# Kernel optimization log

Measured on AMD Instinct MI355X. Metric: run time of the kernel, lower is better.

Reference implementation:

```python
import jax, jax.numpy as jnp
import numpy as np

B, H, W = 8, 64, 64
DIM, NH, WS = 384, 6, 14
HD = DIM // NH
MLP = int(DIM * 4.0)
EPS = 1e-5
SCALE = HD ** -0.5


def setup_inputs() -> dict:
    key = jax.random.key(0)
    ks = jax.random.split(key, 8)
    init = lambda k, shape: (jax.random.normal(k, shape, dtype=jnp.float32) * 0.02)
    return {
        "x": jax.random.normal(ks[0], (B, H, W, DIM), dtype=jnp.float32),
        "ln1_w": jnp.ones((DIM,), jnp.float32),
        "ln1_b": jnp.zeros((DIM,), jnp.float32),
        "qkv_w": init(ks[1], (DIM, 3 * DIM)),
        "qkv_b": jnp.zeros((3 * DIM,), jnp.float32),
        "proj_w": init(ks[2], (DIM, DIM)),
        "proj_b": jnp.zeros((DIM,), jnp.float32),
        "rel_pos_h": init(ks[3], (2 * WS - 1, HD)),
        "rel_pos_w": init(ks[4], (2 * WS - 1, HD)),
        "ln2_w": jnp.ones((DIM,), jnp.float32),
        "ln2_b": jnp.zeros((DIM,), jnp.float32),
        "fc1_w": init(ks[5], (DIM, MLP)),
        "fc1_b": jnp.zeros((MLP,), jnp.float32),
        "fc2_w": init(ks[6], (MLP, DIM)),
        "fc2_b": jnp.zeros((DIM,), jnp.float32),
    }


def _layernorm(x, w, b):
    m = x.mean(-1, keepdims=True)
    v = ((x - m) ** 2).mean(-1, keepdims=True)
    return (x - m) * jax.lax.rsqrt(v + EPS) * w + b


def _get_rel_pos(rel_pos, ws):
    # q_size == k_size == ws and rel_pos has 2*ws-1 rows, so torch's
    # F.interpolate to max_rel_dist=2*ws-1 is an identity; direct indexing.
    coords = jnp.arange(ws)[:, None] - jnp.arange(ws)[None, :] + (ws - 1)
    return rel_pos[coords]  # (ws, ws, head_dim)


def _attention(xw, qkv_w, qkv_b, proj_w, proj_b, rel_pos_h, rel_pos_w):
    Bw = xw.shape[0]
    N = WS * WS
    qkv = xw.reshape(Bw, N, DIM) @ qkv_w + qkv_b  # (Bw, N, 3*DIM)
    qkv = qkv.reshape(Bw, N, 3, NH, HD).transpose(2, 0, 3, 1, 4).reshape(3, Bw * NH, N, HD)
    q, k, v = qkv[0], qkv[1], qkv[2]
    attn = jnp.einsum("bqd,bkd->bqk", q * SCALE, k)  # (Bw*NH, N, N)
    Rh = _get_rel_pos(rel_pos_h, WS)
    Rw = _get_rel_pos(rel_pos_w, WS)
    rq = q.reshape(Bw * NH, WS, WS, HD)
    rel_h = jnp.einsum("bhwc,hkc->bhwk", rq, Rh)
    rel_w = jnp.einsum("bhwc,wkc->bhwk", rq, Rw)
    attn = (attn.reshape(Bw * NH, WS, WS, WS, WS)
            + rel_h[:, :, :, :, None]
            + rel_w[:, :, :, None, :]).reshape(Bw * NH, N, N)
    attn = jax.nn.softmax(attn, axis=-1)
    out = jnp.einsum("bqk,bkd->bqd", attn, v)
    out = out.reshape(Bw, NH, WS, WS, HD).transpose(0, 2, 3, 1, 4).reshape(Bw, WS, WS, DIM)
    return out @ proj_w + proj_b


def reference(x, ln1_w, ln1_b, qkv_w, qkv_b, proj_w, proj_b, rel_pos_h, rel_pos_w,
              ln2_w, ln2_b, fc1_w, fc1_b, fc2_w, fc2_b):
    shortcut = x
    h = _layernorm(x, ln1_w, ln1_b)
    pad_h = (WS - H % WS) % WS
    pad_w = (WS - W % WS) % WS
    Hp, Wp = H + pad_h, W + pad_w
    hp = jnp.pad(h, ((0, 0), (0, pad_h), (0, pad_w), (0, 0)))
    # window partition: (B, Hp, Wp, C) -> (B*nWin, WS, WS, C)
    wins = hp.reshape(B, Hp // WS, WS, Wp // WS, WS, DIM)
    wins = wins.transpose(0, 1, 3, 2, 4, 5).reshape(-1, WS, WS, DIM)
    wins = _attention(wins, qkv_w, qkv_b, proj_w, proj_b, rel_pos_h, rel_pos_w)
    # window unpartition
    y = wins.reshape(B, Hp // WS, Wp // WS, WS, WS, DIM)
    y = y.transpose(0, 1, 3, 2, 4, 5).reshape(B, Hp, Wp, DIM)[:, :H, :W, :]
    x = shortcut + y
    h2 = _layernorm(x, ln2_w, ln2_b)
    mlp = jax.nn.gelu(h2 @ fc1_w + fc1_b, approximate=False) @ fc2_w + fc2_b
    return x + mlp
```

## Files before the change

kernel.cpp:

```cpp
#include <hip/hip_runtime.h>
#include <math.h>

#define DIMC 384
#define NHD  6
#define HD   64
#define WSZ  14
#define NTOK 196
#define NWIN 200
#define NWH  1200
#define MWIN 39200
#define MX   32768
#define MLPD 1536

typedef short short8 __attribute__((ext_vector_type(8)));
typedef float f32x4 __attribute__((ext_vector_type(4)));
typedef float f32x16 __attribute__((ext_vector_type(16)));

__device__ __forceinline__ unsigned short f2bf(float f) {
  unsigned int u = __float_as_uint(f);
  u = (u + 0x7fffu + ((u >> 16) & 1u)) >> 16;
  return (unsigned short)u;
}
__device__ __forceinline__ unsigned int pkbf(float a, float b) {
  unsigned int r; asm("v_cvt_pk_bf16_f32 %0, %1, %2" : "=v"(r) : "v"(a), "v"(b)); return r;
}
__device__ __forceinline__ float gelu_t(float x) {
  float z = 1.5957691216057308f * (x + 0.044715f * x * x * x);
  float e = __expf(z);
  float th = 1.f - 2.f * __builtin_amdgcn_rcpf(e + 1.f);
  return 0.5f * x * (1.f + th);
}

typedef const __attribute__((address_space(1))) unsigned int* gptr_t;
typedef __attribute__((address_space(3))) unsigned int* lptr_t;
__device__ __forceinline__ void gload16(const unsigned short* g, unsigned short* l) {
  __builtin_amdgcn_global_load_lds((gptr_t)(const void*)g, (lptr_t)(void*)l, 16, 0, 0);
}

__global__ void wtrans_kernel(const float* __restrict__ in, unsigned short* __restrict__ out,
                              int K, int N) {
  int id = blockIdx.x * 256 + threadIdx.x;
  if (id >= K * N) return;
  int n = id / K, k = id - n * K;
  out[id] = f2bf(in[(size_t)k * N + n]);
}

__global__ void relprep_kernel(const float* __restrict__ relh, const float* __restrict__ relw,
                               unsigned short* __restrict__ relcat) {
  int id = blockIdx.x * 256 + threadIdx.x;
  if (id >= 64 * 64) return;
  int rc = id >> 6, d = id & 63;
  float v = 0.f;
  if (rc < 27) v = relh[rc * 64 + d] * 8.f;
  else if (rc < 54) v = relw[(rc - 27) * 64 + d] * 8.f;
  relcat[id] = f2bf(v);
}

__global__ void vpad_kernel(unsigned short* __restrict__ vT) {
  int id = blockIdx.x * 256 + threadIdx.x;
  if (id >= 76800 * 3) return;
  int row = id / 3, part = id - row * 3;
  *(int2*)(vT + (size_t)row * 208 + 196 + part * 4) = make_int2(0, 0);
}

__global__ __launch_bounds__(64) void ln1win_kernel(const float* __restrict__ x,
    const float* __restrict__ w, const float* __restrict__ b, unsigned short* __restrict__ xw) {
  int t = blockIdx.x;
  int lane = threadIdx.x;
  int win = t / NTOK, p = t - win * NTOK;
  int bb = win / 25, rem = win - bb * 25;
  int wi = rem / 5, wj = rem - wi * 5;
  int i = p / WSZ, j = p - i * WSZ;
  int r = wi * WSZ + i, c = wj * WSZ + j;
  unsigned short* o = xw + (size_t)t * DIMC;
  if (r >= 64 || c >= 64) {
    #pragma unroll
    for (int q = 0; q < 6; q++) o[lane + q * 64] = 0;
    return;
  }
  const float* xr = x + (((size_t)bb * 64 + r) * 64 + c) * DIMC;
  float v[6]; float s = 0.f, s2 = 0.f;
  #pragma unroll
  for (int q = 0; q < 6; q++) { float f = xr[lane + q * 64]; v[q] = f; s += f; s2 += f * f; }
  #pragma unroll
  for (int off = 32; off; off >>= 1) { s += __shfl_xor(s, off); s2 += __shfl_xor(s2, off); }
  float mean = s * (1.f / DIMC);
  float var  = s2 * (1.f / DIMC) - mean * mean;
  float rstd = rsqrtf(var + 1e-5f);
  #pragma unroll
  for (int q = 0; q < 6; q++) {
    int d = lane + q * 64;
    o[d] = f2bf((v[q] - mean) * rstd * w[d] + b[d]);
  }
}

__global__ __launch_bounds__(64) void ln2_kernel(const float* __restrict__ x2,
    const float* __restrict__ w, const float* __restrict__ b, unsigned short* __restrict__ h2) {
  int t = blockIdx.x; int lane = threadIdx.x;
  const float* xr = x2 + (size_t)t * DIMC;
  unsigned short* o = h2 + (size_t)t * DIMC;
  float v[6]; float s = 0.f, s2 = 0.f;
  #pragma unroll
  for (int q = 0; q < 6; q++) { float f = xr[lane + q * 64]; v[q] = f; s += f; s2 += f * f; }
  #pragma unroll
  for (int off = 32; off; off >>= 1) { s += __shfl_xor(s, off); s2 += __shfl_xor(s2, off); }
  float mean = s * (1.f / DIMC);
  float var  = s2 * (1.f / DIMC) - mean * mean;
  float rstd = rsqrtf(var + 1e-5f);
  #pragma unroll
  for (int q = 0; q < 6; q++) {
    int d = lane + q * 64;
    o[d] = f2bf((v[q] - mean) * rstd * w[d] + b[d]);
  }
}

template <int EPI>
__global__ __launch_bounds__(256) void gemm_kernel(
    const unsigned short* __restrict__ A, const unsigned short* __restrict__ WT,
    int Mrows, int Kd,
    const float* __restrict__ bias, const float* __restrict__ addin,
    float* __restrict__ outf, unsigned short* __restrict__ outb,
    unsigned short* __restrict__ outb2) {
  __shared__ unsigned short As[2][128 * 32];
  __shared__ unsigned short Bs[2][128 * 32];
  const int nwg = gridDim.x * gridDim.y;
  const int flat = blockIdx.y * gridDim.x + blockIdx.x;
  const int xcd = flat & 7, q_ = nwg >> 3, r_ = nwg & 7;
  const int wg = (xcd < r_ ? xcd * (q_ + 1) : r_ * (q_ + 1) + (xcd - r_) * q_) + (flat >> 3);
  const int bx = wg / gridDim.y, by = wg - bx * gridDim.y;
  const int row0 = bx * 128, col0 = by * 128;
  const int tid = threadIdx.x;
  const int l = tid & 63, wid = tid >> 6;
  const int fr = l & 15, fk = (l >> 4) * 8;
  const int wr = (wid >> 1) * 64, wc = (wid & 1) * 64;
  const int sr = l >> 2, sc = (l & 3) * 8;
  const int scs = sc ^ (((sr >> 1) & 3) << 3);
  const int rsw = ((fr >> 1) & 3) << 3;
  f32x4 acc[4][4] = {};
  const unsigned short* ap = A + (size_t)row0 * Kd;
  const unsigned short* bp = WT + (size_t)col0 * Kd;
  const int nt = Kd >> 5;
  #pragma unroll
  for (int j = 0; j < 2; j++) {
    int chunk = j * 4 + wid;
    gload16(ap + (size_t)(chunk * 16 + sr) * Kd + scs, &As[0][chunk * 512]);
    gload16(bp + (size_t)(chunk * 16 + sr) * Kd + scs, &Bs[0][chunk * 512]);
  }
  __syncthreads();
  int cur = 0;
  for (int t = 0; t < nt; ++t) {
    if (t + 1 < nt) {
      const int k0 = (t + 1) * 32;
      #pragma unroll
      for (int j = 0; j < 2; j++) {
        int chunk = j * 4 + wid;
        gload16(ap + (size_t)(chunk * 16 + sr) * Kd + k0 + scs, &As[cur ^ 1][chunk * 512]);
        gload16(bp + (size_t)(chunk * 16 + sr) * Kd + k0 + scs, &Bs[cur ^ 1][chunk * 512]);
      }
    }
    short8 a[4], b[4];
    #pragma unroll
    for (int fi = 0; fi < 4; fi++) {
      a[fi] = *(const short8*)&As[cur][(wr + fi * 16 + fr) * 32 + (fk ^ rsw)];
      b[fi] = *(const short8*)&Bs[cur][(wc + fi * 16 + fr) * 32 + (fk ^ rsw)];
    }
    #pragma unroll
    for (int fi = 0; fi < 4; fi++)
      #pragma unroll
      for (int fj = 0; fj < 4; fj++)
        acc[fi][fj] = __builtin_amdgcn_mfma_f32_16x16x32_bf16(b[fj], a[fi], acc[fi][fj], 0, 0, 0);
    __syncthreads();
    cur ^= 1;
  }
  #pragma unroll
  for (int fi = 0; fi < 4; fi++) {
    const int gr = row0 + wr + fi * 16 + fr;
    if (gr >= Mrows) continue;
    int wv_ = 0, p = 0, valid = 1; size_t pixbase = 0;
    if (EPI == 0 || EPI == 1) { wv_ = gr / NTOK; p = gr - wv_ * NTOK; }
    if (EPI == 1) {
      int bb = wv_ / 25, rem2 = wv_ - bb * 25;
      int wi = rem2 / 5, wj = rem2 - wi * 5;
      int i = p / WSZ, j = p - i * WSZ;
      int rr = wi * WSZ + i, cc = wj * WSZ + j;
      valid = (rr < 64) && (cc < 64);
      pixbase = (((size_t)bb * 64 + rr) * 64 + cc) * DIMC;
    }
    #pragma unroll
    for (int fj = 0; fj < 4; fj++) {
      const int gcb = col0 + wc + fj * 16 + (l >> 4) * 4;
      f32x4 v = acc[fi][fj];
      float4 bv = *(const float4*)&bias[gcb];
      float t0 = v[0] + bv.x, t1 = v[1] + bv.y, t2 = v[2] + bv.z, t3 = v[3] + bv.w;
      if (EPI == 0) {
        int s = gcb / 384, rem = gcb - s * 384;
        int hh = rem >> 6, d0 = gcb & 63;
        int whh = wv_ * NHD + hh;
        if (s == 0) { t0 *= 0.125f; t1 *= 0.125f; t2 *= 0.125f; t3 *= 0.125f; }
        if (s < 2) {
          *(int2*)&outb[((size_t)s * NWH + whh) * (NTOK * 64) + p * 64 + d0] =
              make_int2((int)pkbf(t0, t1), (int)pkbf(t2, t3));
        } else {
          unsigned short* vb = outb2 + ((size_t)whh * 64 + d0) * 208 + p;
          vb[0] = f2bf(t0); vb[208] = f2bf(t1); vb[416] = f2bf(t2); vb[624] = f2bf(t3);
        }
      } else if (EPI == 1) {
        if (valid) {
          size_t idx = pixbase + gcb;
          float4 ad = *(const float4*)&addin[idx];
          *(float4*)&outf[idx] = make_float4(t0 + ad.x, t1 + ad.y, t2 + ad.z, t3 + ad.w);
        }
      } else if (EPI == 2) {
        *(int2*)&outb[(size_t)gr * MLPD + gcb] =
            make_int2((int)pkbf(gelu_t(t0), gelu_t(t1)), (int)pkbf(gelu_t(t2), gelu_t(t3)));
      } else {
        size_t idx = (size_t)gr * DIMC + gcb;
        float4 ad = *(const float4*)&addin[idx];
        *(float4*)&outf[idx] = make_float4(t0 + ad.x, t1 + ad.y, t2 + ad.z, t3 + ad.w);
      }
    }
  }
}

template <bool TAIL>
__device__ __forceinline__ void attn_chunk(
    int kk, int l31, int hi,
    const unsigned short* __restrict__ kg,
    const unsigned short* __restrict__ VT,
    const short8* qf, const short8* qrel,
    f32x16& olo, f32x16& ohi_, float& m_reg, float& s_run) {
  int key = kk * 32 + l31;
  int keyc = (TAIL && key > 195) ? 195 : key;
  f32x16 S = {};
  __builtin_amdgcn_s_setprio(1);
  #pragma unroll
  for (int m = 0; m < 4; m++) {
    short8 kf = *(const short8*)(kg + (size_t)keyc * 64 + m * 16 + hi * 8);
    S = __builtin_amdgcn_mfma_f32_32x32x16_bf16(kf, qf[m], S, 0, 0, 0);
  }
  {
    int ki = keyc / 14, kj = keyc - ki * 14;
    #pragma unroll
    for (int m2 = 0; m2 < 2; m2++) {
      short8 kh;
      #pragma unroll
      for (int j = 0; j < 8; j++) {
        int cc = m2 * 16 + hi * 8 + j;
        kh[j] = (short)((cc == ki || cc == 14 + kj) ? 0x3F80 : 0);
      }
      S = __builtin_amdgcn_mfma_f32_32x32x16_bf16(kh, qrel[m2], S, 0, 0, 0);
    }
  }
  __builtin_amdgcn_s_setprio(0);
  float pmax = -3e38f;
  #pragma unroll
  for (int r = 0; r < 16; r++) {
    if (TAIL) {
      int krow = kk * 32 + (r & 3) + 8 * (r >> 2) + 4 * hi;
      if (krow >= 196) S[r] = -3e38f;
    }
    pmax = fmaxf(pmax, S[r]);
  }
  pmax = fmaxf(pmax, __shfl_xor(pmax, 32));
  if (__any(pmax > m_reg + 8.f)) {
    float m_new = fmaxf(m_reg, pmax);
    float fac = __expf(m_reg - m_new);
    m_reg = m_new;
    s_run *= fac;
    #pragma unroll
    for (int r = 0; r < 16; r++) {
      int qr = (r & 3) + 8 * (r >> 2) + 4 * hi;
      float fr_ = __shfl(fac, qr);
      olo[r] *= fr_; ohi_[r] *= fr_;
    }
  }
  float psum = 0.f;
  #pragma unroll
  for (int r = 0; r < 16; r++) { S[r] = __expf(S[r] - m_reg); psum += S[r]; }
  s_run += psum;
  unsigned int pk[8];
  #pragma unroll
  for (int t = 0; t < 8; t++) pk[t] = pkbf(S[2 * t], S[2 * t + 1]);
  #pragma unroll
  for (int m2 = 0; m2 < 2; m2++) {
    int b_ = m2 * 4;
    unsigned int x0 = (unsigned int)__shfl_xor((int)pk[b_ + 0], 32);
    unsigned int x1 = (unsigned int)__shfl_xor((int)pk[b_ + 1], 32);
    unsigned int x2 = (unsigned int)__shfl_xor((int)pk[b_ + 2], 32);
    unsigned int x3 = (unsigned int)__shfl_xor((int)pk[b_ + 3], 32);
    unsigned int au[4];
    au[0] = hi ? x2 : pk[b_ + 0];
    au[1] = hi ? x3 : pk[b_ + 1];
    au[2] = hi ? pk[b_ + 2] : x0;
    au[3] = hi ? pk[b_ + 3] : x1;
    short8 pa; __builtin_memcpy(&pa, au, 16);
    int kb = kk * 32 + m2 * 16 + hi * 8;
    if (TAIL && kb > 208) kb = 208;
    short8 vblo = *(const short8*)&VT[l31 * 216 + kb];
    short8 vbhi = *(const short8*)&VT[(32 + l31) * 216 + kb];
    __builtin_amdgcn_s_setprio(1);
    olo  = __builtin_amdgcn_mfma_f32_32x32x16_bf16(pa, vblo, olo, 0, 0, 0);
    ohi_ = __builtin_amdgcn_mfma_f32_32x32x16_bf16(pa, vbhi, ohi_, 0, 0, 0);
    __builtin_amdgcn_s_setprio(0);
  }
}

__global__ __launch_bounds__(256) void attn32_kernel(
    const unsigned short* __restrict__ qk_g,
    const unsigned short* __restrict__ vT_g,
    const unsigned short* __restrict__ relcat,
    unsigned short* __restrict__ attnout) {
  __shared__ __align__(16) unsigned short VT[64 * 216];
  __shared__ __align__(16) unsigned short RELB[4][2048];
  const int wh = blockIdx.x;
  const int w = wh / NHD, h = wh - w * NHD;
  const int tid = threadIdx.x;
  const unsigned short* vrow = vT_g + (size_t)wh * 64 * 208;
  for (int e = tid; e < 64 * 27; e += 256) {
    int d = e / 27, c = e - d * 27;
    int4 val = {0, 0, 0, 0};
    if (c < 26) val = *(const int4*)(vrow + d * 208 + c * 8);
    *(int4*)&VT[d * 216 + c * 8] = val;
  }
  __syncthreads();
  const int l = tid & 63, wv = tid >> 6;
  const int l31 = l & 31, hi = l >> 5;
  unsigned short* RB = &RELB[wv][0];
  const unsigned short* qg = qk_g + (size_t)wh * (NTOK * 64);
  const unsigned short* kg = qk_g + (size_t)(NWH + wh) * (NTOK * 64);

  for (int tile = wv; tile < 7; tile += 4) {
    const int q0 = tile * 32;
    int qrow = q0 + l31; if (qrow > 195) qrow = 195;
    short8 qf[4];
    #pragma unroll
    for (int m = 0; m < 4; m++)
      qf[m] = *(const short8*)(qg + (size_t)qrow * 64 + m * 16 + hi * 8);
    #pragma unroll
    for (int rt = 0; rt < 2; rt++) {
      f32x16 cr = {};
      __builtin_amdgcn_s_setprio(1);
      #pragma unroll
      for (int m = 0; m < 4; m++) {
        short8 af = *(const short8*)(relcat + (rt * 32 + l31) * 64 + m * 16 + hi * 8);
        cr = __builtin_amdgcn_mfma_f32_32x32x16_bf16(af, qf[m], cr, 0, 0, 0);
      }
      __builtin_amdgcn_s_setprio(0);
      #pragma unroll
      for (int t = 0; t < 8; t++) {
        int rr = rt * 32 + ((2 * t) & 3) + 8 * (t >> 1) + 4 * hi;
        *(unsigned int*)&RB[l31 * 64 + rr] = pkbf(cr[2 * t], cr[2 * t + 1]);
      }
    }
    __builtin_amdgcn_wave_barrier();
    int qi = qrow / 14, qj = qrow - qi * 14;
    short8 qrel[2];
    #pragma unroll
    for (int m2 = 0; m2 < 2; m2++)
      #pragma unroll
      for (int j = 0; j < 8; j++) {
        int cc = m2 * 16 + hi * 8 + j;
        unsigned short vv = 0;
        if (cc < 14) vv = RB[l31 * 64 + (qi - cc + 13)];
        else if (cc < 28) vv = RB[l31 * 64 + 27 + (qj - (cc - 14) + 13)];
        qrel[m2][j] = (short)vv;
      }
    __builtin_amdgcn_wave_barrier();
    f32x16 olo = {}, ohi_ = {};
    float m_reg = -3e38f, s_run = 0.f;
    for (int kk = 0; kk < 6; kk++)
      attn_chunk<false>(kk, l31, hi, kg, VT, qf, qrel, olo, ohi_, m_reg, s_run);
    attn_chunk<true>(6, l31, hi, kg, VT, qf, qrel, olo, ohi_, m_reg, s_run);
    s_run += __shfl_xor(s_run, 32);
    float inv = 1.f / s_run;
    #pragma unroll
    for (int r = 0; r < 16; r++) {
      int qr = (r & 3) + 8 * (r >> 2) + 4 * hi;
      float ir = __shfl(inv, qr);
      int tok = q0 + qr;
      if (tok < 196) {
        size_t base = ((size_t)w * NTOK + tok) * DIMC + h * 64;
        attnout[base + l31] = f2bf(olo[r] * ir);
        attnout[base + 32 + l31] = f2bf(ohi_[r] * ir);
      }
    }
  }
}

extern "C" void kernel_launch(void* const* d_in, const int* in_sizes, int n_in,
                              void* d_out, int out_size, void* d_ws, size_t ws_size,
                              hipStream_t stream) {
  const float* x     = (const float*)d_in[0];
  const float* ln1w  = (const float*)d_in[1];
  const float* ln1b  = (const float*)d_in[2];
  const float* qkvw  = (const float*)d_in[3];
  const float* qkvb  = (const float*)d_in[4];
  const float* projw = (const float*)d_in[5];
  const float* projb = (const float*)d_in[6];
  const float* relh  = (const float*)d_in[7];
  const float* relw  = (const float*)d_in[8];
  const float* ln2w  = (const float*)d_in[9];
  const float* ln2b  = (const float*)d_in[10];
  const float* fc1w  = (const float*)d_in[11];
  const float* fc1b  = (const float*)d_in[12];
  const float* fc2w  = (const float*)d_in[13];
  const float* fc2b  = (const float*)d_in[14];

  const size_t R0 = 0;
  const size_t R1 = R0 + 50331648;
  const size_t R2 = R1 + 100663296;
  const size_t R3 = R2 + 30105600;
  const size_t NEED = R3 + 3547136;
  if (ws_size < NEED) return;
  char* ws = (char*)d_ws;
  unsigned short* xw     = (unsigned short*)(ws + R0);
  float*          x2     = (float*)(ws + R0);
  unsigned short* qk_g   = (unsigned short*)(ws + R1);
  unsigned short* vT_g   = qk_g + (size_t)2 * NWH * NTOK * 64;
  unsigned short* hidden = (unsigned short*)(ws + R1);
  unsigned short* attno  = (unsigned short*)(ws + R2);
  unsigned short* h2     = (unsigned short*)(ws + R2);
  unsigned short* qkvwT  = (unsigned short*)(ws + R3);
  unsigned short* projwT = qkvwT + 442368;
  unsigned short* fc1wT  = projwT + 147456;
  unsigned short* fc2wT  = fc1wT + 589824;
  unsigned short* relcat = fc2wT + 589824;

  wtrans_kernel<<<1728, 256, 0, stream>>>(qkvw, qkvwT, 384, 1152);
  wtrans_kernel<<<576, 256, 0, stream>>>(projw, projwT, 384, 384);
  wtrans_kernel<<<2304, 256, 0, stream>>>(fc1w, fc1wT, 384, 1536);
  wtrans_kernel<<<2304, 256, 0, stream>>>(fc2w, fc2wT, 1536, 384);
  relprep_kernel<<<16, 256, 0, stream>>>(relh, relw, relcat);
  vpad_kernel<<<900, 256, 0, stream>>>(vT_g);
  ln1win_kernel<<<MWIN, 64, 0, stream>>>(x, ln1w, ln1b, xw);
  gemm_kernel<0><<<dim3(307, 9), 256, 0, stream>>>(xw, qkvwT, MWIN, 384, qkvb, nullptr, nullptr, qk_g, vT_g);
  attn32_kernel<<<NWH, 256, 0, stream>>>(qk_g, vT_g, relcat, attno);
  gemm_kernel<1><<<dim3(307, 3), 256, 0, stream>>>(attno, projwT, MWIN, 384, projb, x, x2, nullptr, nullptr);
  ln2_kernel<<<MX, 64, 0, stream>>>(x2, ln2w, ln2b, h2);
  gemm_kernel<2><<<dim3(256, 12), 256, 0, stream>>>(h2, fc1wT, MX, 384, fc1b, nullptr, nullptr, hidden, nullptr);
  gemm_kernel<3><<<dim3(256, 3), 256, 0, stream>>>(hidden, fc2wT, MX, 1536, fc2b, x2, (float*)d_out, nullptr, nullptr);
}
```

Measured before the change: 361.2 us.

## Triple-buffer GEMM LDS with two-stage prefetch and single barrier per k-step

Moves the bf16 GEMM main loop from double to triple buffering in shared memory, prefetching two k-tiles ahead. Explicit vmcnt waits and one barrier per iteration replace the trailing __syncthreads, so global loads stay in flight across iterations. It also raises wave priority around the MFMA block with s_setprio. LDS use grows by half, which may lower occupancy, and the hand-written waitcnt counts depend on gload16 issuing exactly four vector memory ops per stage.

```diff
diff --git a/kernel.cpp b/kernel.cpp
--- a/kernel.cpp
+++ b/kernel.cpp
@@ -121,8 +121,8 @@
     const float* __restrict__ bias, const float* __restrict__ addin,
     float* __restrict__ outf, unsigned short* __restrict__ outb,
     unsigned short* __restrict__ outb2) {
-  __shared__ unsigned short As[2][128 * 32];
-  __shared__ unsigned short Bs[2][128 * 32];
+  __shared__ unsigned short As[3][128 * 32];
+  __shared__ unsigned short Bs[3][128 * 32];
   const int nwg = gridDim.x * gridDim.y;
   const int flat = blockIdx.y * gridDim.x + blockIdx.x;
   const int xcd = flat & 7, q_ = nwg >> 3, r_ = nwg & 7;
@@ -140,37 +140,41 @@
   const unsigned short* ap = A + (size_t)row0 * Kd;
   const unsigned short* bp = WT + (size_t)col0 * Kd;
   const int nt = Kd >> 5;
-  #pragma unroll
-  for (int j = 0; j < 2; j++) {
-    int chunk = j * 4 + wid;
-    gload16(ap + (size_t)(chunk * 16 + sr) * Kd + scs, &As[0][chunk * 512]);
-    gload16(bp + (size_t)(chunk * 16 + sr) * Kd + scs, &Bs[0][chunk * 512]);
-  }
-  __syncthreads();
-  int cur = 0;
+
+  auto stage = [&](int t, int b) {
+    const int k0 = t * 32;
+    #pragma unroll
+    for (int j = 0; j < 2; j++) {
+      int chunk = j * 4 + wid;
+      gload16(ap + (size_t)(chunk * 16 + sr) * Kd + k0 + scs, &As[b][chunk * 512]);
+      gload16(bp + (size_t)(chunk * 16 + sr) * Kd + k0 + scs, &Bs[b][chunk * 512]);
+    }
+  };
+  stage(0, 0);
+  stage(1, 1);
+  int c = 0;
   for (int t = 0; t < nt; ++t) {
-    if (t + 1 < nt) {
-      const int k0 = (t + 1) * 32;
-      #pragma unroll
-      for (int j = 0; j < 2; j++) {
-        int chunk = j * 4 + wid;
-        gload16(ap + (size_t)(chunk * 16 + sr) * Kd + k0 + scs, &As[cur ^ 1][chunk * 512]);
-        gload16(bp + (size_t)(chunk * 16 + sr) * Kd + k0 + scs, &Bs[cur ^ 1][chunk * 512]);
-      }
-    }
+    if (t < nt - 1) asm volatile("s_waitcnt vmcnt(4)" ::: "memory");
+    else            asm volatile("s_waitcnt vmcnt(0)" ::: "memory");
+    __builtin_amdgcn_s_barrier();
+    __builtin_amdgcn_sched_barrier(0);
+    if (t + 2 < nt) stage(t + 2, (c + 2 >= 3) ? c - 1 : c + 2);
     short8 a[4], b[4];
     #pragma unroll
     for (int fi = 0; fi < 4; fi++) {
-      a[fi] = *(const short8*)&As[cur][(wr + fi * 16 + fr) * 32 + (fk ^ rsw)];
-      b[fi] = *(const short8*)&Bs[cur][(wc + fi * 16 + fr) * 32 + (fk ^ rsw)];
-    }
+      a[fi] = *(const short8*)&As[c][(wr + fi * 16 + fr) * 32 + (fk ^ rsw)];
+      b[fi] = *(const short8*)&Bs[c][(wc + fi * 16 + fr) * 32 + (fk ^ rsw)];
+    }
+    asm volatile("s_waitcnt lgkmcnt(0)" ::: "memory");
+    __builtin_amdgcn_sched_barrier(0);
+    __builtin_amdgcn_s_setprio(1);
     #pragma unroll
     for (int fi = 0; fi < 4; fi++)
       #pragma unroll
       for (int fj = 0; fj < 4; fj++)
         acc[fi][fj] = __builtin_amdgcn_mfma_f32_16x16x32_bf16(b[fj], a[fi], acc[fi][fj], 0, 0, 0);
-    __syncthreads();
-    cur ^= 1;
+    __builtin_amdgcn_s_setprio(0);
+    c = (c + 1 >= 3) ? 0 : c + 1;
   }
   #pragma unroll
   for (int fi = 0; fi < 4; fi++) {
```

Result: no change. 358.1 us (-0.9%).
